# Kernel tuning notes

Hardware: AMD Instinct MI355X
Metric: run time of the kernel (lower is better)

## Reference

```python
import jax, jax.numpy as jnp
import numpy as np

N = 1024
INTER_CH = 10      # C(4,2) + (8-4)
HIDDEN_CH = 32
OUT_CH = 1
THRESH = 4
TOP_K = 8
INTERACT = 4


def setup_inputs() -> dict:
    key = jax.random.key(0)
    k1, k2, k3, k4, k5 = jax.random.split(key, 5)
    x = jax.random.normal(k1, (16, N, N), dtype=jnp.float32)
    is_active_flags = jnp.ones((16,), dtype=bool)
    # 1x1 conv params (stored as dense matrices; kernel_size=1)
    w1 = jax.random.normal(k2, (HIDDEN_CH, INTER_CH), dtype=jnp.float32) / np.sqrt(INTER_CH)
    b1 = jax.random.normal(k3, (HIDDEN_CH, 1, 1), dtype=jnp.float32) * 0.01
    w2 = jax.random.normal(k4, (OUT_CH, HIDDEN_CH), dtype=jnp.float32) / np.sqrt(HIDDEN_CH)
    b2 = jax.random.normal(k5, (OUT_CH, 1, 1), dtype=jnp.float32) * 0.01
    return {"x": x, "is_active_flags": is_active_flags, "w1": w1, "b1": b1, "w2": w2, "b2": b2}


def reference(x, is_active_flags, w1, b1, w2, b2):
    gate_active = jnp.sum(is_active_flags) >= THRESH

    def _active_path(operand):
        inputs, mask = operand                       # (16, n, n), (16,)
        _, slogdet = jnp.linalg.slogdet(inputs)      # (16,)
        scores = jnp.where(mask, slogdet, -jnp.inf)
        _, indices = jax.lax.top_k(scores, TOP_K)
        top_x = inputs[indices]                      # (8, n, n)
        top_interact_x = top_x[:INTERACT]            # (4, n, n)
        next_preserve_x = top_x[INTERACT:]           # (4, n, n)
        idx1, idx2 = jnp.triu_indices(INTERACT, k=1)  # 6 pairs
        pairs = jnp.matmul(top_interact_x[idx1], top_interact_x[idx2])  # (6, n, n)
        concat = jnp.concatenate([pairs, next_preserve_x], axis=0)      # (10, n, n)
        hidden = jnp.einsum('oc,chw->ohw', w1, concat) + b1             # 1x1 conv
        out = jnp.einsum('oc,chw->ohw', w2, hidden) + b2                # 1x1 conv
        return (out, jnp.array(True))

    def _inactive_path(operand):
        inputs, _ = operand
        _, n, m = inputs.shape
        return (jnp.zeros((OUT_CH, n, m), dtype=jnp.float32), jnp.array(False))

    out, out_active = jax.lax.cond(gate_active, _active_path, _inactive_path, (x, is_active_flags))
    return (out, out_active)
```

## Files before the change

### kernel.cpp

```cpp
#include <hip/hip_runtime.h>
#include <math.h>

#define N 1024
#define NN (N*N)
#define PST 36

__global__ void init_kernel(double* scores) {
  int t = threadIdx.x;
  if (t < 16) scores[t] = 0.0;
}

__global__ __launch_bounds__(256) void copy_kernel(const float4* __restrict__ src,
                                                   float4* __restrict__ dst) {
  int i = blockIdx.x * 256 + threadIdx.x;
  dst[i] = src[i];
}

__global__ __launch_bounds__(256, 1) void panel_kernel(float* __restrict__ lu,
                                                       int* __restrict__ ipiv,
                                                       double* __restrict__ scores,
                                                       int c0) {
  __shared__ __align__(16) float sh[1024 * PST];
  __shared__ float ujjS[32];
  __shared__ float redv[4];
  __shared__ int   redk[4];
  const int m = blockIdx.x;
  float* A = lu + (size_t)m * NN;
  const int R = N - c0;
  const int tid = threadIdx.x;

  for (int idx = tid; idx < (R << 3); idx += 256) {
    int r = idx >> 3, q = idx & 7;
    *(float4*)&sh[r * PST + 4 * q] =
        *(const float4*)(A + (size_t)(c0 + r) * N + c0 + 4 * q);
  }
  __syncthreads();

  int pcur;
  {
    float bval = -1.0f; int brow = 0x7fffffff;
    #pragma unroll
    for (int t4 = 0; t4 < 4; ++t4) {
      int r = tid + (t4 << 8);
      if (r < R) {
        float v = fabsf(sh[r * PST]);
        if (v > bval || (v == bval && r < brow)) { bval = v; brow = r; }
      }
    }
    #pragma unroll
    for (int mask = 32; mask; mask >>= 1) {
      float ov = __shfl_xor(bval, mask);
      int   orr = __shfl_xor(brow, mask);
      if (ov > bval || (ov == bval && orr < brow)) { bval = ov; brow = orr; }
    }
    if ((tid & 63) == 0) { redv[tid >> 6] = bval; redk[tid >> 6] = brow; }
    __syncthreads();
    float bv = redv[0]; int bk = redk[0];
    float v1 = redv[1]; int k1 = redk[1];
    float v2 = redv[2]; int k2 = redk[2];
    float v3 = redv[3]; int k3 = redk[3];
    if (v1 > bv || (v1 == bv && k1 < bk)) { bv = v1; bk = k1; }
    if (v2 > bv || (v2 == bv && k2 < bk)) { bv = v2; bk = k2; }
    if (v3 > bv || (v3 == bv && k3 < bk)) { bv = v3; bk = k3; }
    pcur = bk;
  }
  __syncthreads();

  #pragma unroll 1
  for (int j = 0; j < 32; ++j) {
    if (pcur != j && tid < 8) {
      float4 a = *(float4*)&sh[j * PST + 4 * tid];
      float4 b = *(float4*)&sh[pcur * PST + 4 * tid];
      *(float4*)&sh[j * PST + 4 * tid] = b;
      *(float4*)&sh[pcur * PST + 4 * tid] = a;
    }
    if (tid == 0) ipiv[m * 32 + j] = c0 + pcur;
    __syncthreads();

    const int qj = j >> 2, ej = j & 3;
    const int jn = j + 1;
    const int qn = (j < 31) ? (jn >> 2) : -1, en = jn & 3;
    const float ujj = sh[j * PST + j];
    if (tid == 0) ujjS[j] = ujj;
    const float rujj = 1.0f / ujj;

    float4 u4[8];
    #pragma unroll
    for (int q = 0; q < 8; ++q)
      if (4 * q + 3 >= j) u4[q] = *(const float4*)&sh[j * PST + 4 * q];

    float bval = -1.0f; int brow = 0x7fffffff;
    #pragma unroll
    for (int t4 = 0; t4 < 4; ++t4) {
      int r = tid + (t4 << 8);
      if (r > j && r < R) {
        float* rp = &sh[r * PST];
        float l = 0.0f, nv = 0.0f;
        #pragma unroll
        for (int q = 0; q < 8; ++q) {
          if (q < qj) continue;
          float4 v = *(float4*)&rp[4 * q];
          if (q == qj) {
            float aj = (ej == 0) ? v.x : (ej == 1) ? v.y : (ej == 2) ? v.z : v.w;
            l = aj * rujj;
            if (ej == 0)      { v.x = l; v.y -= l * u4[q].y; v.z -= l * u4[q].z; v.w -= l * u4[q].w; }
            else if (ej == 1) { v.y = l; v.z -= l * u4[q].z; v.w -= l * u4[q].w; }
            else if (ej == 2) { v.z = l; v.w -= l * u4[q].w; }
            else              { v.w = l; }
          } else {
            v.x -= l * u4[q].x; v.y -= l * u4[q].y;
            v.z -= l * u4[q].z; v.w -= l * u4[q].w;
          }
          if (q == qn)
            nv = (en == 0) ? v.x : (en == 1) ? v.y : (en == 2) ? v.z : v.w;
          *(float4*)&rp[4 * q] = v;
        }
        if (j < 31) {
          float av = fabsf(nv);
          if (av > bval || (av == bval && r < brow)) { bval = av; brow = r; }
        }
      }
    }
    if (j < 31) {
      #pragma unroll
      for (int mask = 32; mask; mask >>= 1) {
        float ov = __shfl_xor(bval, mask);
        int   orr = __shfl_xor(brow, mask);
        if (ov > bval || (ov == bval && orr < brow)) { bval = ov; brow = orr; }
      }
      if ((tid & 63) == 0) { redv[tid >> 6] = bval; redk[tid >> 6] = brow; }
    }
    __syncthreads();
    if (j < 31) {
      float bv = redv[0]; int bk = redk[0];
      float v1 = redv[1]; int k1 = redk[1];
      float v2 = redv[2]; int k2 = redk[2];
      float v3 = redv[3]; int k3 = redk[3];
      if (v1 > bv || (v1 == bv && k1 < bk)) { bv = v1; bk = k1; }
      if (v2 > bv || (v2 == bv && k2 < bk)) { bv = v2; bk = k2; }
      if (v3 > bv || (v3 == bv && k3 < bk)) { bv = v3; bk = k3; }
      pcur = bk;
    }
  }

  for (int idx = tid; idx < (R << 3); idx += 256) {
    int r = idx >> 3, q = idx & 7;
    *(float4*)(A + (size_t)(c0 + r) * N + c0 + 4 * q) =
        *(const float4*)&sh[r * PST + 4 * q];
  }
  if (tid < 64) {
    double lg = 0.0;
    if (tid < 32) lg = log(fabs((double)ujjS[tid]));
    #pragma unroll
    for (int mask = 32; mask; mask >>= 1) lg += __shfl_xor(lg, mask);
    if (tid == 0) atomicAdd(&scores[m], lg);
  }
}

__global__ __launch_bounds__(256) void ptrsm_kernel(float* __restrict__ lu,
                                                    const int* __restrict__ ipiv,
                                                    int c0, int ncs) {
  const int m  = blockIdx.x / ncs;
  const int cs = blockIdx.x % ncs;
  const int s0 = c0 + 32 + cs * 256;
  const int tid = threadIdx.x;
  const int col = s0 + tid;
  const bool ac = col < N;
  float* A = lu + (size_t)m * NN;
  const int R = N - c0;
  __shared__ int   rowAt[1024];
  __shared__ float L11s[32][33];
  __shared__ int   dDst[48];
  __shared__ int   dSrc[48];
  __shared__ int   dcount;

  for (int r = tid; r < R; r += 256) rowAt[r] = c0 + r;
  if (tid == 0) dcount = 0;
  for (int idx = tid; idx < 1024; idx += 256) {
    int i = idx >> 5, k = idx & 31;
    L11s[i][k] = A[(size_t)(c0 + i) * N + c0 + k];
  }
  __syncthreads();
  if (tid == 0) {
    #pragma unroll 1
    for (int j = 0; j < 32; ++j) {
      int p = ipiv[m * 32 + j];
      if (p != c0 + j) { int t = rowAt[j]; rowAt[j] = rowAt[p - c0]; rowAt[p - c0] = t; }
    }
  }
  __syncthreads();
  for (int r = 32 + tid; r < R; r += 256) {
    if (rowAt[r] != c0 + r) {
      int i = atomicAdd(&dcount, 1);
      dDst[i] = c0 + r; dSrc[i] = rowAt[r];
    }
  }
  __syncthreads();
  const int nd = dcount;

  float pay[32];
  #pragma unroll
  for (int i = 0; i < 32; ++i)
    if (i < nd && ac) pay[i] = A[(size_t)dSrc[i] * N + col];
  float u[32];
  #pragma unroll
  for (int i = 0; i < 32; ++i)
    if (ac) u[i] = A[(size_t)rowAt[i] * N + col];

  #pragma unroll
  for (int i = 1; i < 32; ++i) {
    float a = u[i];
    #pragma unroll
    for (int k = 0; k < 32; ++k)
      if (k < i) a -= L11s[i][k] * u[k];
    u[i] = a;
  }

  #pragma unroll
  for (int i = 0; i < 32; ++i)
    if (i < nd && ac) A[(size_t)dDst[i] * N + col] = pay[i];
  #pragma unroll
  for (int i = 0; i < 32; ++i)
    if (ac) A[(size_t)(c0 + i) * N + col] = u[i];
}

__global__ __launch_bounds__(256) void update_kernel(float* __restrict__ lu,
                                                     int c0, int nrt, int ncs) {
  const int per = nrt * ncs;
  const int m  = blockIdx.x / per;
  const int t  = blockIdx.x % per;
  const int rt = t / ncs, cs = t % ncs;
  const int r0 = c0 + 32 + rt * 64;
  const int s0 = c0 + 32 + cs * 256;
  const int tid = threadIdx.x;
  float* A = lu + (size_t)m * NN;
  __shared__ float Lts[32][68];
  __shared__ float Us[32][260];
  for (int idx = tid; idx < 2048; idx += 256) {
    int r = idx >> 5, k = idx & 31;
    Lts[k][r] = (r0 + r < N) ? A[(size_t)(r0 + r) * N + c0 + k] : 0.0f;
  }
  for (int idx = tid; idx < 8192; idx += 256) {
    int k = idx >> 8, c = idx & 255;
    Us[k][c] = (s0 + c < N) ? A[(size_t)(c0 + k) * N + s0 + c] : 0.0f;
  }
  __syncthreads();
  const int tx = tid & 63;
  const int ty = tid >> 6;
  float4 acc[16];
  #pragma unroll
  for (int e = 0; e < 16; ++e) acc[e] = make_float4(0.f, 0.f, 0.f, 0.f);
  #pragma unroll 4
  for (int k = 0; k < 32; ++k) {
    float4 b  = *(const float4*)&Us[k][tx * 4];
    float4 a0 = *(const float4*)&Lts[k][ty * 16 + 0];
    float4 a1 = *(const float4*)&Lts[k][ty * 16 + 4];
    float4 a2 = *(const float4*)&Lts[k][ty * 16 + 8];
    float4 a3 = *(const float4*)&Lts[k][ty * 16 + 12];
    acc[0].x  += a0.x*b.x; acc[0].y  += a0.x*b.y; acc[0].z  += a0.x*b.z; acc[0].w  += a0.x*b.w;
    acc[1].x  += a0.y*b.x; acc[1].y  += a0.y*b.y; acc[1].z  += a0.y*b.z; acc[1].w  += a0.y*b.w;
    acc[2].x  += a0.z*b.x; acc[2].y  += a0.z*b.y; acc[2].z  += a0.z*b.z; acc[2].w  += a0.z*b.w;
    acc[3].x  += a0.w*b.x; acc[3].y  += a0.w*b.y; acc[3].z  += a0.w*b.z; acc[3].w  += a0.w*b.w;
    acc[4].x  += a1.x*b.x; acc[4].y  += a1.x*b.y; acc[4].z  += a1.x*b.z; acc[4].w  += a1.x*b.w;
    acc[5].x  += a1.y*b.x; acc[5].y  += a1.y*b.y; acc[5].z  += a1.y*b.z; acc[5].w  += a1.y*b.w;
    acc[6].x  += a1.z*b.x; acc[6].y  += a1.z*b.y; acc[6].z  += a1.z*b.z; acc[6].w  += a1.z*b.w;
    acc[7].x  += a1.w*b.x; acc[7].y  += a1.w*b.y; acc[7].z  += a1.w*b.z; acc[7].w  += a1.w*b.w;
    acc[8].x  += a2.x*b.x; acc[8].y  += a2.x*b.y; acc[8].z  += a2.x*b.z; acc[8].w  += a2.x*b.w;
    acc[9].x  += a2.y*b.x; acc[9].y  += a2.y*b.y; acc[9].z  += a2.y*b.z; acc[9].w  += a2.y*b.w;
    acc[10].x += a2.z*b.x; acc[10].y += a2.z*b.y; acc[10].z += a2.z*b.z; acc[10].w += a2.z*b.w;
    acc[11].x += a2.w*b.x; acc[11].y += a2.w*b.y; acc[11].z += a2.w*b.z; acc[11].w += a2.w*b.w;
    acc[12].x += a3.x*b.x; acc[12].y += a3.x*b.y; acc[12].z += a3.x*b.z; acc[12].w += a3.x*b.w;
    acc[13].x += a3.y*b.x; acc[13].y += a3.y*b.y; acc[13].z += a3.y*b.z; acc[13].w += a3.y*b.w;
    acc[14].x += a3.z*b.x; acc[14].y += a3.z*b.y; acc[14].z += a3.z*b.z; acc[14].w += a3.z*b.w;
    acc[15].x += a3.w*b.x; acc[15].y += a3.w*b.y; acc[15].z += a3.w*b.z; acc[15].w += a3.w*b.w;
  }
  const bool colok = (s0 + tx * 4) < N;
  #pragma unroll
  for (int e = 0; e < 16; ++e) {
    int r = r0 + ty * 16 + e;
    if (r < N && colok) {
      float4* p = (float4*)&A[(size_t)r * N + s0 + tx * 4];
      float4 v = *p;
      v.x -= acc[e].x; v.y -= acc[e].y; v.z -= acc[e].z; v.w -= acc[e].w;
      *p = v;
    }
  }
}

__global__ void select_kernel(const void* __restrict__ flagsraw, const double* __restrict__ scores,
                              const float* __restrict__ w1, const float* __restrict__ b1,
                              const float* __restrict__ w2, const float* __restrict__ b2,
                              int* __restrict__ topidx, float* __restrict__ misc,
                              float* __restrict__ out_tail) {
  if (threadIdx.x != 0 || blockIdx.x != 0) return;
  const unsigned char* fb = (const unsigned char*)flagsraw;
  bool nonbin = false, off4 = false;
  for (int i = 0; i < 16; ++i) {
    if (fb[i] > 1) nonbin = true;
    if ((i & 3) && fb[i]) off4 = true;
  }
  int f[16]; int nact = 0;
  for (int i = 0; i < 16; ++i) {
    int v;
    if (nonbin)      v = (((const float*)flagsraw)[i] != 0.0f);
    else if (off4)   v = (fb[i] != 0);
    else             v = (((const int*)flagsraw)[i] != 0);
    f[i] = v; nact += v;
  }
  int gate = (nact >= 4) ? 1 : 0;
  double sc[16];
  for (int i = 0; i < 16; ++i) sc[i] = f[i] ? scores[i] : -1.0e300;
  bool used[16] = {};
  for (int k = 0; k < 8; ++k) {
    int bi = -1; double bv = 0.0;
    for (int i = 0; i < 16; ++i)
      if (!used[i] && (bi < 0 || sc[i] > bv)) { bv = sc[i]; bi = i; }
    used[bi] = true;
    topidx[k] = bi;
  }
  for (int cC = 0; cC < 10; ++cC) {
    float s = 0.0f;
    for (int h = 0; h < 32; ++h) s += w2[h] * w1[h * 10 + cC];
    misc[cC] = s;
  }
  float be = 0.0f;
  for (int h = 0; h < 32; ++h) be += w2[h] * b1[h];
  be += b2[0];
  misc[10] = be;
  ((int*)misc)[12] = gate;
  *out_tail = gate ? 1.0f : 0.0f;
}

__global__ __launch_bounds__(256) void build_m_kernel(const float* __restrict__ x,
                                                      const int* __restrict__ topidx,
                                                      const float* __restrict__ misc,
                                                      float* __restrict__ M) {
  int i = blockIdx.x * 256 + threadIdx.x;
  const float4* T1 = (const float4*)(x + (size_t)topidx[1] * NN);
  const float4* T2 = (const float4*)(x + (size_t)topidx[2] * NN);
  const float4* T3 = (const float4*)(x + (size_t)topidx[3] * NN);
  float w0 = misc[0], w1_ = misc[1], w2_ = misc[2], w3_ = misc[3], w4_ = misc[4], w5_ = misc[5];
  float4 t1 = T1[i], t2 = T2[i], t3 = T3[i];
  float4 m0, m1, m2;
  m0.x = w0 * t1.x + w1_ * t2.x + w2_ * t3.x;
  m0.y = w0 * t1.y + w1_ * t2.y + w2_ * t3.y;
  m0.z = w0 * t1.z + w1_ * t2.z + w2_ * t3.z;
  m0.w = w0 * t1.w + w1_ * t2.w + w2_ * t3.w;
  m1.x = w3_ * t2.x + w4_ * t3.x;
  m1.y = w3_ * t2.y + w4_ * t3.y;
  m1.z = w3_ * t2.z + w4_ * t3.z;
  m1.w = w3_ * t2.w + w4_ * t3.w;
  m2.x = w5_ * t3.x;  m2.y = w5_ * t3.y;  m2.z = w5_ * t3.z;  m2.w = w5_ * t3.w;
  ((float4*)M)[i] = m0;
  ((float4*)(M + NN))[i] = m1;
  ((float4*)(M + 2 * (size_t)NN))[i] = m2;
}

__global__ __launch_bounds__(256) void final_gemm_kernel(const float* __restrict__ x,
                                                         const float* __restrict__ M,
                                                         const int* __restrict__ topidx,
                                                         float* __restrict__ P) {
  const int chunk = blockIdx.x >> 8;
  const int t  = blockIdx.x & 255;
  const int tr = t >> 4, tc = t & 15;
  const int mi  = chunk >> 1;
  const int k0b = (chunk & 1) << 9;
  const float* A = x + (size_t)topidx[mi] * NN;
  const float* B = M + (size_t)mi * NN;
  __shared__ float As[32][68];
  __shared__ float Bs[32][68];
  const int ty = threadIdx.x >> 4, tx = threadIdx.x & 15;
  float acc[4][4] = {};
  for (int k0 = k0b; k0 < k0b + 512; k0 += 32) {
    for (int idx = threadIdx.x; idx < 2048; idx += 256) {
      int r = idx >> 5, k = idx & 31;
      As[k][r] = A[(size_t)(tr * 64 + r) * N + k0 + k];
    }
    for (int idx = threadIdx.x; idx < 2048; idx += 256) {
      int k = idx >> 6, cc = idx & 63;
      Bs[k][cc] = B[(size_t)(k0 + k) * N + tc * 64 + cc];
    }
    __syncthreads();
    #pragma unroll 8
    for (int k = 0; k < 32; ++k) {
      float4 a = *(const float4*)&As[k][ty * 4];
      float4 b = *(const float4*)&Bs[k][tx * 4];
      acc[0][0] += a.x * b.x; acc[0][1] += a.x * b.y; acc[0][2] += a.x * b.z; acc[0][3] += a.x * b.w;
      acc[1][0] += a.y * b.x; acc[1][1] += a.y * b.y; acc[1][2] += a.y * b.z; acc[1][3] += a.y * b.w;
      acc[2][0] += a.z * b.x; acc[2][1] += a.z * b.y; acc[2][2] += a.z * b.z; acc[2][3] += a.z * b.w;
      acc[3][0] += a.w * b.x; acc[3][1] += a.w * b.y; acc[3][2] += a.w * b.z; acc[3][3] += a.w * b.w;
    }
    __syncthreads();
  }
  float* Pc = P + (size_t)chunk * NN;
  #pragma unroll
  for (int i = 0; i < 4; ++i) {
    size_t r = (size_t)(tr * 64 + ty * 4 + i);
    float4 v = make_float4(acc[i][0], acc[i][1], acc[i][2], acc[i][3]);
    *(float4*)&Pc[r * N + tc * 64 + tx * 4] = v;
  }
}

__global__ __launch_bounds__(256) void reduce_out_kernel(const float* __restrict__ x,
                                                         const float* __restrict__ P,
                                                         const int* __restrict__ topidx,
                                                         const float* __restrict__ misc,
                                                         float* __restrict__ out) {
  int i = blockIdx.x * 256 + threadIdx.x;
  int gate = ((const int*)misc)[12];
  float4* o = (float4*)out;
  if (!gate) { o[i] = make_float4(0.f, 0.f, 0.f, 0.f); return; }
  float w6 = misc[6], w7 = misc[7], w8 = misc[8], w9 = misc[9], be = misc[10];
  float4 p0 = ((const float4*)(x + (size_t)topidx[4] * NN))[i];
  float4 p1 = ((const float4*)(x + (size_t)topidx[5] * NN))[i];
  float4 p2 = ((const float4*)(x + (size_t)topidx[6] * NN))[i];
  float4 p3 = ((const float4*)(x + (size_t)topidx[7] * NN))[i];
  float4 r;
  r.x = be + w6 * p0.x + w7 * p1.x + w8 * p2.x + w9 * p3.x;
  r.y = be + w6 * p0.y + w7 * p1.y + w8 * p2.y + w9 * p3.y;
  r.z = be + w6 * p0.z + w7 * p1.z + w8 * p2.z + w9 * p3.z;
  r.w = be + w6 * p0.w + w7 * p1.w + w8 * p2.w + w9 * p3.w;
  #pragma unroll
  for (int cN = 0; cN < 6; ++cN) {
    float4 q = ((const float4*)(P + (size_t)cN * NN))[i];
    r.x += q.x; r.y += q.y; r.z += q.z; r.w += q.w;
  }
  o[i] = r;
}

extern "C" void kernel_launch(void* const* d_in, const int* in_sizes, int n_in,
                              void* d_out, int out_size, void* d_ws, size_t ws_size,
                              hipStream_t stream) {
  const float* x  = (const float*)d_in[0];
  const void*  fl = d_in[1];
  const float* w1 = (const float*)d_in[2];
  const float* b1 = (const float*)d_in[3];
  const float* w2 = (const float*)d_in[4];
  const float* b2 = (const float*)d_in[5];
  float* out = (float*)d_out;

  char* ws = (char*)d_ws;
  float* LU = (float*)ws;
  float* Mm = (float*)ws;
  float* P  = (float*)(ws + (size_t)12 * 1024 * 1024);
  size_t tail = (size_t)16 * NN * sizeof(float);
  double* scores = (double*)(ws + tail);
  int*    ipiv   = (int*)(ws + tail + 256);
  int*    topidx = (int*)(ws + tail + 256 + 2304);
  float*  misc   = (float*)(ws + tail + 256 + 2304 + 256);

  init_kernel<<<1, 64, 0, stream>>>(scores);
  copy_kernel<<<16384, 256, 0, stream>>>((const float4*)x, (float4*)LU);

  for (int c0 = 0; c0 < N; c0 += 32) {
    panel_kernel<<<16, 256, 0, stream>>>(LU, ipiv, scores, c0);
    int tcols = N - c0 - 32;
    if (tcols > 0) {
      int ncs = (tcols + 255) / 256;
      ptrsm_kernel<<<16 * ncs, 256, 0, stream>>>(LU, ipiv, c0, ncs);
      int nrt = (tcols + 63) / 64;
      update_kernel<<<16 * nrt * ncs, 256, 0, stream>>>(LU, c0, nrt, ncs);
    }
  }

  select_kernel<<<1, 64, 0, stream>>>(fl, scores, w1, b1, w2, b2, topidx, misc, out + NN);
  build_m_kernel<<<1024, 256, 0, stream>>>(x, topidx, misc, Mm);
  final_gemm_kernel<<<1536, 256, 0, stream>>>(x, Mm, topidx, P);
  reduce_out_kernel<<<1024, 256, 0, stream>>>(x, P, topidx, misc, out);
}
```

Measured before the change: 4.201 ms.

## Keep panel rows in registers and track pivots via a permutation array

The panel factorization now holds each thread's rows in registers instead of a 144 KB shared-memory tile. Pivoting no longer swaps rows physically: it records a row permutation that the trsm and update kernels read indirectly. The pivot-selection reduction is double-buffered so each column step needs one fewer barrier. The aim is to cut shared-memory traffic and barriers on the serial panel critical path, at the cost of many registers per thread (row[4][8] float4) and gathered, non-contiguous row reads in the later kernels.

```diff
diff --git a/kernel.cpp b/kernel.cpp
--- a/kernel.cpp
+++ b/kernel.cpp
@@ -3,7 +3,6 @@
 
 #define N 1024
 #define NN (N*N)
-#define PST 36
 
 __global__ void init_kernel(double* scores) {
   int t = threadIdx.x;
@@ -17,33 +16,41 @@
 }
 
 __global__ __launch_bounds__(256, 1) void panel_kernel(float* __restrict__ lu,
-                                                       int* __restrict__ ipiv,
+                                                       unsigned short* __restrict__ rowsrc,
                                                        double* __restrict__ scores,
                                                        int c0) {
-  __shared__ __align__(16) float sh[1024 * PST];
+  __shared__ __align__(16) float prow[32];
   __shared__ float ujjS[32];
-  __shared__ float redv[4];
-  __shared__ int   redk[4];
+  __shared__ float redv[2][4];
+  __shared__ int   redk[2][4];
+  __shared__ int Vv[1024];
+  __shared__ int Pv[1024];
   const int m = blockIdx.x;
   float* A = lu + (size_t)m * NN;
   const int R = N - c0;
   const int tid = threadIdx.x;
 
-  for (int idx = tid; idx < (R << 3); idx += 256) {
-    int r = idx >> 3, q = idx & 7;
-    *(float4*)&sh[r * PST + 4 * q] =
-        *(const float4*)(A + (size_t)(c0 + r) * N + c0 + 4 * q);
-  }
-  __syncthreads();
-
-  int pcur;
+  float4 row[4][8] = {};
+  unsigned actm = 0u;
+  #pragma unroll
+  for (int k = 0; k < 4; ++k) {
+    int r = tid + (k << 8);
+    if (r < R) {
+      actm |= (1u << k);
+      const float* src = A + (size_t)(c0 + r) * N + c0;
+      #pragma unroll
+      for (int q = 0; q < 8; ++q) row[k][q] = *(const float4*)(src + 4 * q);
+    }
+  }
+  for (int i = tid; i < R; i += 256) { Vv[i] = i; Pv[i] = i; }
+
   {
     float bval = -1.0f; int brow = 0x7fffffff;
     #pragma unroll
-    for (int t4 = 0; t4 < 4; ++t4) {
-      int r = tid + (t4 << 8);
-      if (r < R) {
-        float v = fabsf(sh[r * PST]);
+    for (int k = 0; k < 4; ++k) {
+      if ((actm >> k) & 1u) {
+        int r = tid + (k << 8);
+        float v = fabsf(row[k][0].x);
         if (v > bval || (v == bval && r < brow)) { bval = v; brow = r; }
       }
     }
@@ -53,53 +60,67 @@
       int   orr = __shfl_xor(brow, mask);
       if (ov > bval || (ov == bval && orr < brow)) { bval = ov; brow = orr; }
     }
-    if ((tid & 63) == 0) { redv[tid >> 6] = bval; redk[tid >> 6] = brow; }
-    __syncthreads();
-    float bv = redv[0]; int bk = redk[0];
-    float v1 = redv[1]; int k1 = redk[1];
-    float v2 = redv[2]; int k2 = redk[2];
-    float v3 = redv[3]; int k3 = redk[3];
-    if (v1 > bv || (v1 == bv && k1 < bk)) { bv = v1; bk = k1; }
-    if (v2 > bv || (v2 == bv && k2 < bk)) { bv = v2; bk = k2; }
-    if (v3 > bv || (v3 == bv && k3 < bk)) { bv = v3; bk = k3; }
-    pcur = bk;
+    if ((tid & 63) == 0) { redv[0][tid >> 6] = bval; redk[0][tid >> 6] = brow; }
   }
   __syncthreads();
 
   #pragma unroll 1
   for (int j = 0; j < 32; ++j) {
-    if (pcur != j && tid < 8) {
-      float4 a = *(float4*)&sh[j * PST + 4 * tid];
-      float4 b = *(float4*)&sh[pcur * PST + 4 * tid];
-      *(float4*)&sh[j * PST + 4 * tid] = b;
-      *(float4*)&sh[pcur * PST + 4 * tid] = a;
-    }
-    if (tid == 0) ipiv[m * 32 + j] = c0 + pcur;
+    int pcur;
+    {
+      const int pb = j & 1;
+      float bv = redv[pb][0]; int bk = redk[pb][0];
+      float v1 = redv[pb][1]; int k1 = redk[pb][1];
+      float v2 = redv[pb][2]; int k2 = redk[pb][2];
+      float v3 = redv[pb][3]; int k3 = redk[pb][3];
+      if (v1 > bv || (v1 == bv && k1 < bk)) { bv = v1; bk = k1; }
+      if (v2 > bv || (v2 == bv && k2 < bk)) { bv = v2; bk = k2; }
+      if (v3 > bv || (v3 == bv && k3 < bk)) { bv = v3; bk = k3; }
+      pcur = bk;
+    }
+    if (tid == (pcur & 255)) {
+      const int kk = pcur >> 8;
+      float4* pd = (float4*)prow;
+      #pragma unroll
+      for (int q = 0; q < 8; ++q) {
+        float4 v = row[0][q];
+        if (kk == 1) v = row[1][q];
+        if (kk == 2) v = row[2][q];
+        if (kk == 3) v = row[3][q];
+        pd[q] = v;
+      }
+      actm &= ~(1u << kk);
+    }
+    if (tid == 0) {
+      int b  = Pv[pcur];
+      int pa = Vv[j];
+      Vv[j] = pcur; Vv[b] = pa;
+      Pv[pcur] = j; Pv[pa] = b;
+    }
     __syncthreads();
 
+    const float ujj = prow[j];
+    if (tid == 0) ujjS[j] = ujj;
+    const float rujj = 1.0f / ujj;
     const int qj = j >> 2, ej = j & 3;
     const int jn = j + 1;
     const int qn = (j < 31) ? (jn >> 2) : -1, en = jn & 3;
-    const float ujj = sh[j * PST + j];
-    if (tid == 0) ujjS[j] = ujj;
-    const float rujj = 1.0f / ujj;
 
     float4 u4[8];
     #pragma unroll
     for (int q = 0; q < 8; ++q)
-      if (4 * q + 3 >= j) u4[q] = *(const float4*)&sh[j * PST + 4 * q];
+      if (4 * q + 3 >= j) u4[q] = *(const float4*)&prow[4 * q];
 
     float bval = -1.0f; int brow = 0x7fffffff;
     #pragma unroll
-    for (int t4 = 0; t4 < 4; ++t4) {
-      int r = tid + (t4 << 8);
-      if (r > j && r < R) {
-        float* rp = &sh[r * PST];
+    for (int k = 0; k < 4; ++k) {
+      if ((actm >> k) & 1u) {
+        const int r = tid + (k << 8);
         float l = 0.0f, nv = 0.0f;
         #pragma unroll
         for (int q = 0; q < 8; ++q) {
           if (q < qj) continue;
-          float4 v = *(float4*)&rp[4 * q];
+          float4 v = row[k][q];
           if (q == qj) {
             float aj = (ej == 0) ? v.x : (ej == 1) ? v.y : (ej == 2) ? v.z : v.w;
             l = aj * rujj;
@@ -113,7 +134,7 @@
           }
           if (q == qn)
             nv = (en == 0) ? v.x : (en == 1) ? v.y : (en == 2) ? v.z : v.w;
-          *(float4*)&rp[4 * q] = v;
+          row[k][q] = v;
         }
         if (j < 31) {
           float av = fabsf(nv);
@@ -128,26 +149,21 @@
         int   orr = __shfl_xor(brow, mask);
         if (ov > bval || (ov == bval && orr < brow)) { bval = ov; brow = orr; }
       }
-      if ((tid & 63) == 0) { redv[tid >> 6] = bval; redk[tid >> 6] = brow; }
+      if ((tid & 63) == 0) { redv[jn & 1][tid >> 6] = bval; redk[jn & 1][tid >> 6] = brow; }
     }
     __syncthreads();
-    if (j < 31) {
-      float bv = redv[0]; int bk = redk[0];
-      float v1 = redv[1]; int k1 = redk[1];
-      float v2 = redv[2]; int k2 = redk[2];
-      float v3 = redv[3]; int k3 = redk[3];
-      if (v1 > bv || (v1 == bv && k1 < bk)) { bv = v1; bk = k1; }
-      if (v2 > bv || (v2 == bv && k2 < bk)) { bv = v2; bk = k2; }
-      if (v3 > bv || (v3 == bv && k3 < bk)) { bv = v3; bk = k3; }
-      pcur = bk;
-    }
-  }
-
-  for (int idx = tid; idx < (R << 3); idx += 256) {
-    int r = idx >> 3, q = idx & 7;
-    *(float4*)(A + (size_t)(c0 + r) * N + c0 + 4 * q) =
-        *(const float4*)&sh[r * PST + 4 * q];
-  }
+  }
+
+  #pragma unroll
+  for (int k = 0; k < 4; ++k) {
+    int r = tid + (k << 8);
+    if (r < R) {
+      float* dst = A + (size_t)(c0 + r) * N + c0;
+      #pragma unroll
+      for (int q = 0; q < 8; ++q) *(float4*)(dst + 4 * q) = row[k][q];
+    }
+  }
+  for (int i = tid; i < R; i += 256) rowsrc[m * 1024 + i] = (unsigned short)(c0 + Vv[i]);
   if (tid < 64) {
     double lg = 0.0;
     if (tid < 32) lg = log(fabs((double)ujjS[tid]));
@@ -158,7 +174,7 @@
 }
 
 __global__ __launch_bounds__(256) void ptrsm_kernel(float* __restrict__ lu,
-                                                    const int* __restrict__ ipiv,
+                                                    const unsigned short* __restrict__ rowsrc,
                                                     int c0, int ncs) {
   const int m  = blockIdx.x / ncs;
   const int cs = blockIdx.x % ncs;
@@ -174,21 +190,13 @@
   __shared__ int   dSrc[48];
   __shared__ int   dcount;
 
-  for (int r = tid; r < R; r += 256) rowAt[r] = c0 + r;
+  for (int r = tid; r < R; r += 256) rowAt[r] = (int)rowsrc[m * 1024 + r];
   if (tid == 0) dcount = 0;
+  __syncthreads();
   for (int idx = tid; idx < 1024; idx += 256) {
     int i = idx >> 5, k = idx & 31;
-    L11s[i][k] = A[(size_t)(c0 + i) * N + c0 + k];
-  }
-  __syncthreads();
-  if (tid == 0) {
-    #pragma unroll 1
-    for (int j = 0; j < 32; ++j) {
-      int p = ipiv[m * 32 + j];
-      if (p != c0 + j) { int t = rowAt[j]; rowAt[j] = rowAt[p - c0]; rowAt[p - c0] = t; }
-    }
-  }
-  __syncthreads();
+    L11s[i][k] = A[(size_t)rowAt[i] * N + c0 + k];
+  }
   for (int r = 32 + tid; r < R; r += 256) {
     if (rowAt[r] != c0 + r) {
       int i = atomicAdd(&dcount, 1);
@@ -225,6 +233,7 @@
 }
 
 __global__ __launch_bounds__(256) void update_kernel(float* __restrict__ lu,
+                                                     const unsigned short* __restrict__ rowsrc,
                                                      int c0, int nrt, int ncs) {
   const int per = nrt * ncs;
   const int m  = blockIdx.x / per;
@@ -238,7 +247,8 @@
   __shared__ float Us[32][260];
   for (int idx = tid; idx < 2048; idx += 256) {
     int r = idx >> 5, k = idx & 31;
-    Lts[k][r] = (r0 + r < N) ? A[(size_t)(r0 + r) * N + c0 + k] : 0.0f;
+    int rr = r0 + r;
+    Lts[k][r] = (rr < N) ? A[(size_t)rowsrc[m * 1024 + rr - c0] * N + c0 + k] : 0.0f;
   }
   for (int idx = tid; idx < 8192; idx += 256) {
     int k = idx >> 8, c = idx & 255;
@@ -445,21 +455,21 @@
   float* P  = (float*)(ws + (size_t)12 * 1024 * 1024);
   size_t tail = (size_t)16 * NN * sizeof(float);
   double* scores = (double*)(ws + tail);
-  int*    ipiv   = (int*)(ws + tail + 256);
-  int*    topidx = (int*)(ws + tail + 256 + 2304);
-  float*  misc   = (float*)(ws + tail + 256 + 2304 + 256);
+  unsigned short* rowsrc = (unsigned short*)(ws + tail + 256);
+  int*    topidx = (int*)(ws + tail + 256 + 32768);
+  float*  misc   = (float*)(ws + tail + 256 + 32768 + 256);
 
   init_kernel<<<1, 64, 0, stream>>>(scores);
   copy_kernel<<<16384, 256, 0, stream>>>((const float4*)x, (float4*)LU);
 
   for (int c0 = 0; c0 < N; c0 += 32) {
-    panel_kernel<<<16, 256, 0, stream>>>(LU, ipiv, scores, c0);
+    panel_kernel<<<16, 256, 0, stream>>>(LU, rowsrc, scores, c0);
     int tcols = N - c0 - 32;
     if (tcols > 0) {
       int ncs = (tcols + 255) / 256;
-      ptrsm_kernel<<<16 * ncs, 256, 0, stream>>>(LU, ipiv, c0, ncs);
+      ptrsm_kernel<<<16 * ncs, 256, 0, stream>>>(LU, rowsrc, c0, ncs);
       int nrt = (tcols + 63) / 64;
-      update_kernel<<<16 * nrt * ncs, 256, 0, stream>>>(LU, c0, nrt, ncs);
+      update_kernel<<<16 * nrt * ncs, 256, 0, stream>>>(LU, rowsrc, c0, nrt, ncs);
     }
   }
 
```

Result: slower. 6.930 ms (+65.0%).
